# Kernel optimization log

Measured on AMD Instinct MI355X. Metric: run time of the kernel, lower is better.

The kernel has to match this reference:

```python
import jax, jax.numpy as jnp
import numpy as np

B, T, I, H, O = 64, 512, 256, 1024, 128

def setup_inputs() -> dict:
    key = jax.random.key(0)
    ks = jax.random.split(key, 7)
    s_ih = 1.0 / np.sqrt(H)
    return {
        "x":    jax.random.normal(ks[0], (B, T, I), dtype=jnp.float32),
        "W_ih": jax.random.uniform(ks[1], (H, I), minval=-s_ih, maxval=s_ih, dtype=jnp.float32),
        "W_hh": jax.random.uniform(ks[2], (H, H), minval=-s_ih, maxval=s_ih, dtype=jnp.float32),
        "b_ih": jax.random.uniform(ks[3], (H,), minval=-s_ih, maxval=s_ih, dtype=jnp.float32),
        "b_hh": jax.random.uniform(ks[4], (H,), minval=-s_ih, maxval=s_ih, dtype=jnp.float32),
        "W_lin": jax.random.uniform(ks[5], (O, H), minval=-s_ih, maxval=s_ih, dtype=jnp.float32),
        "b_lin": jax.random.uniform(ks[6], (O,), minval=-s_ih, maxval=s_ih, dtype=jnp.float32),
    }

def reference(x, W_ih, W_hh, b_ih, b_hh, W_lin, b_lin):
    # Precompute input projections for all timesteps: [T, B, H]
    xp = jnp.einsum('bti,hi->tbh', x, W_ih) + b_ih + b_hh
    h0 = jnp.zeros((x.shape[0], W_hh.shape[0]), dtype=x.dtype)

    def step(h, xp_t):
        h_new = jnp.tanh(xp_t + h @ W_hh.T)
        return h_new, None

    h_last, _ = jax.lax.scan(step, h0, xp)
    # Final linear on last hidden state: [B, O]
    return h_last @ W_lin.T + b_lin
```

## Files before the change

kernel.cpp:

```cpp
#include <hip/hip_runtime.h>
#include <cstdint>
#include <cstddef>

#define B_ 64
#define T_ 512
#define I_ 256
#define H_ 1024
#define O_ 128

#define NGRP  8
#define NSLC  8
#define GROWS 8
#define SCOLS 128

typedef __attribute__((ext_vector_type(8))) short short8;
typedef __attribute__((ext_vector_type(4))) float f32x4;

__device__ __forceinline__ unsigned short f2bf(float f) {
    union { float f; unsigned int u; } v; v.f = f;
    unsigned int r = v.u + 0x7fffu + ((v.u >> 16) & 1u);
    return (unsigned short)(r >> 16);
}
__device__ __forceinline__ float bf2f(unsigned short h) {
    union { float f; unsigned int u; } v; v.u = ((unsigned int)h) << 16;
    return v.f;
}
__device__ __forceinline__ short8 pack8(const float* p) {
    float4 a = *(const float4*)p;
    float4 b = *(const float4*)(p + 4);
    short8 r;
    r[0] = (short)f2bf(a.x); r[1] = (short)f2bf(a.y);
    r[2] = (short)f2bf(a.z); r[3] = (short)f2bf(a.w);
    r[4] = (short)f2bf(b.x); r[5] = (short)f2bf(b.y);
    r[6] = (short)f2bf(b.z); r[7] = (short)f2bf(b.w);
    return r;
}
__device__ __forceinline__ f32x4 zero4() {
    f32x4 v; v[0] = 0.f; v[1] = 0.f; v[2] = 0.f; v[3] = 0.f; return v;
}
__device__ __forceinline__ void vdrain() {
    asm volatile("s_waitcnt vmcnt(0)" ::: "memory");
}

#define XS 264

__global__ __launch_bounds__(256) void xproj_kernel(
        const float* __restrict__ x, const float* __restrict__ W_ih,
        const float* __restrict__ b_ih, const float* __restrict__ b_hh,
        unsigned short* __restrict__ xp) {
    const int ntile = blockIdx.x;
    const int tg    = blockIdx.y;
    const int tid   = threadIdx.x;
    const int wave  = tid >> 6, lane = tid & 63;
    const int m     = lane & 15, quad = lane >> 4;
    const int wrow  = (wave & 1) * 32;
    const int wcol  = (wave >> 1) * 32;

    __shared__ unsigned short lds_x[64 * XS];

    short8 bfr[2][8];
    float  bias[2];
    #pragma unroll
    for (int ct = 0; ct < 2; ++ct) {
        const int col = ntile * 64 + wcol + ct * 16 + m;
        bias[ct] = b_ih[col] + b_hh[col];
        #pragma unroll
        for (int ks = 0; ks < 8; ++ks)
            bfr[ct][ks] = pack8(W_ih + (size_t)col * I_ + ks * 32 + quad * 8);
    }

    for (int it = 0; it < 8; ++it) {
        const int t = tg * 8 + it;
        #pragma unroll
        for (int j = 0; j < 16; ++j) {
            const int row = j * 4 + wave;
            float4 v = *(const float4*)(x + ((size_t)row * T_ + t) * I_ + lane * 4);
            uint2 p;
            p.x = (unsigned)f2bf(v.x) | ((unsigned)f2bf(v.y) << 16);
            p.y = (unsigned)f2bf(v.z) | ((unsigned)f2bf(v.w) << 16);
            *(uint2*)(&lds_x[row * XS + lane * 4]) = p;
        }
        __syncthreads();

        f32x4 acc[2][2];
        #pragma unroll
        for (int i = 0; i < 2; ++i)
            #pragma unroll
            for (int j = 0; j < 2; ++j) acc[i][j] = zero4();

        #pragma unroll
        for (int ks = 0; ks < 8; ++ks) {
            const int kb = ks * 32 + quad * 8;
            short8 af[2];
            #pragma unroll
            for (int rt = 0; rt < 2; ++rt)
                af[rt] = *(const short8*)(&lds_x[(wrow + rt * 16 + m) * XS + kb]);
            #pragma unroll
            for (int rt = 0; rt < 2; ++rt)
                #pragma unroll
                for (int ct = 0; ct < 2; ++ct)
                    acc[rt][ct] = __builtin_amdgcn_mfma_f32_16x16x32_bf16(
                        af[rt], bfr[ct][ks], acc[rt][ct], 0, 0, 0);
        }

        #pragma unroll
        for (int ct = 0; ct < 2; ++ct) {
            const int col = ntile * 64 + wcol + ct * 16 + m;
            #pragma unroll
            for (int rt = 0; rt < 2; ++rt)
                #pragma unroll
                for (int r = 0; r < 4; ++r) {
                    const int bl = wrow + rt * 16 + quad * 4 + r;
                    xp[((size_t)t * B_ + bl) * H_ + col] =
                        f2bf(acc[rt][ct][r] + bias[ct]);
                }
        }
        __syncthreads();
    }
}

#define LDS_STRIDE 1032
#define PO_S 20
#define POLL_BOUND 4096

__global__ __launch_bounds__(512, 1) void rnn_kernel(
        const float* __restrict__ W_hh, const unsigned short* __restrict__ xp,
        unsigned short* __restrict__ hbuf, unsigned int* __restrict__ flags) {
    const int slice = blockIdx.x >> 3;
    const int group = blockIdx.x & 7;
    const int tid   = threadIdx.x;
    const int wave  = tid >> 6, lane = tid & 63;
    const int m     = lane & 15, quad = lane >> 4;
    const int col   = slice * SCOLS + wave * 16 + m;

    __shared__ unsigned short lds_h[GROWS * LDS_STRIDE];
    __shared__ unsigned short lds_po[8][GROWS * PO_S];

    short8 bfrag[32];
    #pragma unroll
    for (int ks = 0; ks < 32; ++ks)
        bfrag[ks] = pack8(W_hh + (size_t)col * H_ + ks * 32 + quad * 8);

    unsigned int* gflags = flags + group * 8;
    unsigned int* myflag = gflags + slice;
    const unsigned int* pollp = gflags + (lane & 7);
    unsigned short* lds_po_w = &lds_po[wave][0];

    const int srow = tid >> 6, useg = tid & 63;
    const int prow = lane >> 3, pseg = lane & 7;

    for (int t = 0; t < T_; ++t) {
        const unsigned short* hsrc = hbuf + (size_t)(t & 1) * (B_ * H_)
                                          + (size_t)group * GROWS * H_;
        unsigned short* hdst = hbuf + (size_t)((t + 1) & 1) * (B_ * H_);

        unsigned short xpv[4];
        {
            const unsigned short* xpp =
                xp + ((size_t)t * B_ + group * GROWS + (quad & 1) * 4) * H_ + col;
            #pragma unroll
            for (int r = 0; r < 4; ++r) xpv[r] = xpp[(size_t)r * H_];
        }

        if (t > 0) {
            if (wave == 0) {
                const unsigned target = (unsigned)t;
                int spins = 0;
                while (true) {
                    unsigned fv;
                    asm volatile(
                        "global_load_dword %0, %1, off sc0 sc1\n\t"
                        "s_waitcnt vmcnt(0)"
                        : "=v"(fv) : "v"(pollp) : "memory");
                    if (__ballot(fv >= target) == ~0ull) break;
                    if (++spins >= POLL_BOUND) break;
                }
            }
            __syncthreads();
        }

        {
            const unsigned short* rp = hsrc + (size_t)srow * H_;
            uint4 sv0, sv1;
            asm volatile("global_load_dwordx4 %0, %1, off sc0 sc1"
                         : "=v"(sv0) : "v"(rp + useg * 8) : "memory");
            asm volatile("global_load_dwordx4 %0, %1, off sc0 sc1"
                         : "=v"(sv1) : "v"(rp + (useg + 64) * 8) : "memory");
            vdrain();
            *(uint4*)(&lds_h[srow * LDS_STRIDE + useg * 8]) = sv0;
            *(uint4*)(&lds_h[srow * LDS_STRIDE + (useg + 64) * 8]) = sv1;
        }
        __syncthreads();

        f32x4 acc[4];
        #pragma unroll
        for (int j = 0; j < 4; ++j) acc[j] = zero4();
        #pragma unroll
        for (int ks = 0; ks < 32; ks += 4) {
            #pragma unroll
            for (int j = 0; j < 4; ++j) {
                short8 a = *(const short8*)(
                    &lds_h[(m & 7) * LDS_STRIDE + (ks + j) * 32 + quad * 8]);
                acc[j] = __builtin_amdgcn_mfma_f32_16x16x32_bf16(
                    a, bfrag[ks + j], acc[j], 0, 0, 0);
            }
        }

        if (quad < 2) {
            #pragma unroll
            for (int r = 0; r < 4; ++r) {
                float v = acc[0][r] + acc[1][r] + acc[2][r] + acc[3][r]
                        + bf2f(xpv[r]);
                v = tanhf(v);
                lds_po_w[(quad * 4 + r) * PO_S + m] = f2bf(v);
            }
        }
        {
            unsigned v = *(const unsigned*)(&lds_po_w[prow * PO_S + pseg * 2]);
            const void* p = hdst + (size_t)(group * GROWS + prow) * H_
                            + slice * SCOLS + wave * 16 + pseg * 2;
            asm volatile("global_store_dword %0, %1, off sc0 sc1"
                         :: "v"(p), "v"(v) : "memory");
            vdrain();
        }
        __syncthreads();
        if (tid == 0 && t < T_ - 1) {
            unsigned fv = (unsigned)(t + 1);
            asm volatile("global_store_dword %0, %1, off sc0 sc1"
                         :: "v"(myflag), "v"(fv) : "memory");
        }
    }
}

__global__ __launch_bounds__(256) void out_kernel(
        const unsigned short* __restrict__ hfinal, const float* __restrict__ W_lin,
        const float* __restrict__ b_lin, float* __restrict__ out) {
    const int gwave = (int)((blockIdx.x * 256 + threadIdx.x) >> 6);
    const int lane  = threadIdx.x & 63;
    const int b = gwave >> 7, o = gwave & 127;

    const unsigned short* hp = hfinal + (size_t)b * H_ + lane * 16;
    const float*          wp = W_lin  + (size_t)o * H_ + lane * 16;
    float s = 0.f;
    #pragma unroll
    for (int j = 0; j < 16; ++j) s += bf2f(hp[j]) * wp[j];
    #pragma unroll
    for (int d = 32; d > 0; d >>= 1) s += __shfl_down(s, d, 64);
    if (lane == 0) out[(size_t)b * O_ + o] = s + b_lin[o];
}

extern "C" void kernel_launch(void* const* d_in, const int* in_sizes, int n_in,
                              void* d_out, int out_size, void* d_ws, size_t ws_size,
                              hipStream_t stream) {
    const float* x     = (const float*)d_in[0];
    const float* W_ih  = (const float*)d_in[1];
    const float* W_hh  = (const float*)d_in[2];
    const float* b_ih  = (const float*)d_in[3];
    const float* b_hh  = (const float*)d_in[4];
    const float* W_lin = (const float*)d_in[5];
    const float* b_lin = (const float*)d_in[6];

    const size_t XP_ELEMS = (size_t)T_ * B_ * H_;
    unsigned short* xp    = (unsigned short*)d_ws;
    unsigned short* hbuf  = xp + XP_ELEMS;
    unsigned int*   flags = (unsigned int*)(hbuf + 2 * (size_t)B_ * H_);

    (void)hipMemsetAsync(hbuf, 0,
                         2 * (size_t)B_ * H_ * sizeof(unsigned short)
                         + NGRP * 64 * sizeof(unsigned int), stream);

    dim3 gA(H_ / 64, T_ / 8);
    xproj_kernel<<<gA, 256, 0, stream>>>(x, W_ih, b_ih, b_hh, xp);
    rnn_kernel<<<64, 512, 0, stream>>>(W_hh, xp, hbuf, flags);
    out_kernel<<<(B_ * O_) / 4, 256, 0, stream>>>(hbuf, W_lin, b_lin, (float*)d_out);
}
```

Before: 1.785 ms.

## Fuse input projection into persistent RNN kernel with double-buffered x staging

Removes the separate xproj kernel and its bf16 intermediate buffer (T*B*H). Each RNN block now computes its slice of x_t @ W_ih^T with MFMA every step, using W_ih fragments held in registers. It prefetches the next timestep's x rows into a double-buffered LDS tile alongside the h loads. This avoids writing and re-reading the intermediate and the extra launch, but adds per-step MFMA work and register pressure to the latency-bound recurrent loop.

```diff
diff --git a/kernel.cpp b/kernel.cpp
--- a/kernel.cpp
+++ b/kernel.cpp
@@ -42,89 +42,15 @@
     asm volatile("s_waitcnt vmcnt(0)" ::: "memory");
 }
 
-#define XS 264
-
-__global__ __launch_bounds__(256) void xproj_kernel(
-        const float* __restrict__ x, const float* __restrict__ W_ih,
-        const float* __restrict__ b_ih, const float* __restrict__ b_hh,
-        unsigned short* __restrict__ xp) {
-    const int ntile = blockIdx.x;
-    const int tg    = blockIdx.y;
-    const int tid   = threadIdx.x;
-    const int wave  = tid >> 6, lane = tid & 63;
-    const int m     = lane & 15, quad = lane >> 4;
-    const int wrow  = (wave & 1) * 32;
-    const int wcol  = (wave >> 1) * 32;
-
-    __shared__ unsigned short lds_x[64 * XS];
-
-    short8 bfr[2][8];
-    float  bias[2];
-    #pragma unroll
-    for (int ct = 0; ct < 2; ++ct) {
-        const int col = ntile * 64 + wcol + ct * 16 + m;
-        bias[ct] = b_ih[col] + b_hh[col];
-        #pragma unroll
-        for (int ks = 0; ks < 8; ++ks)
-            bfr[ct][ks] = pack8(W_ih + (size_t)col * I_ + ks * 32 + quad * 8);
-    }
-
-    for (int it = 0; it < 8; ++it) {
-        const int t = tg * 8 + it;
-        #pragma unroll
-        for (int j = 0; j < 16; ++j) {
-            const int row = j * 4 + wave;
-            float4 v = *(const float4*)(x + ((size_t)row * T_ + t) * I_ + lane * 4);
-            uint2 p;
-            p.x = (unsigned)f2bf(v.x) | ((unsigned)f2bf(v.y) << 16);
-            p.y = (unsigned)f2bf(v.z) | ((unsigned)f2bf(v.w) << 16);
-            *(uint2*)(&lds_x[row * XS + lane * 4]) = p;
-        }
-        __syncthreads();
-
-        f32x4 acc[2][2];
-        #pragma unroll
-        for (int i = 0; i < 2; ++i)
-            #pragma unroll
-            for (int j = 0; j < 2; ++j) acc[i][j] = zero4();
-
-        #pragma unroll
-        for (int ks = 0; ks < 8; ++ks) {
-            const int kb = ks * 32 + quad * 8;
-            short8 af[2];
-            #pragma unroll
-            for (int rt = 0; rt < 2; ++rt)
-                af[rt] = *(const short8*)(&lds_x[(wrow + rt * 16 + m) * XS + kb]);
-            #pragma unroll
-            for (int rt = 0; rt < 2; ++rt)
-                #pragma unroll
-                for (int ct = 0; ct < 2; ++ct)
-                    acc[rt][ct] = __builtin_amdgcn_mfma_f32_16x16x32_bf16(
-                        af[rt], bfr[ct][ks], acc[rt][ct], 0, 0, 0);
-        }
-
-        #pragma unroll
-        for (int ct = 0; ct < 2; ++ct) {
-            const int col = ntile * 64 + wcol + ct * 16 + m;
-            #pragma unroll
-            for (int rt = 0; rt < 2; ++rt)
-                #pragma unroll
-                for (int r = 0; r < 4; ++r) {
-                    const int bl = wrow + rt * 16 + quad * 4 + r;
-                    xp[((size_t)t * B_ + bl) * H_ + col] =
-                        f2bf(acc[rt][ct][r] + bias[ct]);
-                }
-        }
-        __syncthreads();
-    }
-}
-
 #define LDS_STRIDE 1032
+#define XSL 264
 #define PO_S 20
 #define POLL_BOUND 4096
 
 __global__ __launch_bounds__(512, 1) void rnn_kernel(
-        const float* __restrict__ W_hh, const unsigned short* __restrict__ xp,
+        const float* __restrict__ W_hh, const float* __restrict__ W_ih,
+        const float* __restrict__ b_ih, const float* __restrict__ b_hh,
+        const float* __restrict__ x,
         unsigned short* __restrict__ hbuf, unsigned int* __restrict__ flags) {
     const int slice = blockIdx.x >> 3;
     const int group = blockIdx.x & 7;
@@ -135,11 +61,17 @@
 
     __shared__ unsigned short lds_h[GROWS * LDS_STRIDE];
     __shared__ unsigned short lds_po[8][GROWS * PO_S];
+    __shared__ unsigned short lds_x2[2][GROWS * XSL];
 
     short8 bfrag[32];
     #pragma unroll
     for (int ks = 0; ks < 32; ++ks)
         bfrag[ks] = pack8(W_hh + (size_t)col * H_ + ks * 32 + quad * 8);
+    short8 bfragIH[8];
+    #pragma unroll
+    for (int ks = 0; ks < 8; ++ks)
+        bfragIH[ks] = pack8(W_ih + (size_t)col * I_ + ks * 32 + quad * 8);
+    const float biasc = b_ih[col] + b_hh[col];
 
     unsigned int* gflags = flags + group * 8;
     unsigned int* myflag = gflags + slice;
@@ -149,17 +81,28 @@
     const int srow = tid >> 6, useg = tid & 63;
     const int prow = lane >> 3, pseg = lane & 7;
 
+    {
+        float4 v = *(const float4*)(
+            x + ((size_t)(group * GROWS + srow) * T_ + 0) * I_ + useg * 4);
+        uint2 p;
+        p.x = (unsigned)f2bf(v.x) | ((unsigned)f2bf(v.y) << 16);
+        p.y = (unsigned)f2bf(v.z) | ((unsigned)f2bf(v.w) << 16);
+        *(uint2*)(&lds_x2[0][srow * XSL + useg * 4]) = p;
+    }
+    __syncthreads();
+
     for (int t = 0; t < T_; ++t) {
         const unsigned short* hsrc = hbuf + (size_t)(t & 1) * (B_ * H_)
                                           + (size_t)group * GROWS * H_;
         unsigned short* hdst = hbuf + (size_t)((t + 1) & 1) * (B_ * H_);
 
-        unsigned short xpv[4];
-        {
-            const unsigned short* xpp =
-                xp + ((size_t)t * B_ + group * GROWS + (quad & 1) * 4) * H_ + col;
-            #pragma unroll
-            for (int r = 0; r < 4; ++r) xpv[r] = xpp[(size_t)r * H_];
+        f32x4 axp = zero4();
+        #pragma unroll
+        for (int ks = 0; ks < 8; ++ks) {
+            short8 a = *(const short8*)(
+                &lds_x2[t & 1][(m & 7) * XSL + ks * 32 + quad * 8]);
+            axp = __builtin_amdgcn_mfma_f32_16x16x32_bf16(
+                a, bfragIH[ks], axp, 0, 0, 0);
         }
 
         if (t > 0) {
@@ -186,6 +129,15 @@
                          : "=v"(sv0) : "v"(rp + useg * 8) : "memory");
             asm volatile("global_load_dwordx4 %0, %1, off sc0 sc1"
                          : "=v"(sv1) : "v"(rp + (useg + 64) * 8) : "memory");
+            if (t + 1 < T_) {
+                float4 v = *(const float4*)(
+                    x + ((size_t)(group * GROWS + srow) * T_ + (t + 1)) * I_
+                      + useg * 4);
+                uint2 p;
+                p.x = (unsigned)f2bf(v.x) | ((unsigned)f2bf(v.y) << 16);
+                p.y = (unsigned)f2bf(v.z) | ((unsigned)f2bf(v.w) << 16);
+                *(uint2*)(&lds_x2[(t + 1) & 1][srow * XSL + useg * 4]) = p;
+            }
             vdrain();
             *(uint4*)(&lds_h[srow * LDS_STRIDE + useg * 8]) = sv0;
             *(uint4*)(&lds_h[srow * LDS_STRIDE + (useg + 64) * 8]) = sv1;
@@ -210,7 +162,7 @@
             #pragma unroll
             for (int r = 0; r < 4; ++r) {
                 float v = acc[0][r] + acc[1][r] + acc[2][r] + acc[3][r]
-                        + bf2f(xpv[r]);
+                        + axp[r] + biasc;
                 v = tanhf(v);
                 lds_po_w[(quad * 4 + r) * PO_S + m] = f2bf(v);
             }
@@ -260,17 +212,13 @@
     const float* W_lin = (const float*)d_in[5];
     const float* b_lin = (const float*)d_in[6];
 
-    const size_t XP_ELEMS = (size_t)T_ * B_ * H_;
-    unsigned short* xp    = (unsigned short*)d_ws;
-    unsigned short* hbuf  = xp + XP_ELEMS;
+    unsigned short* hbuf  = (unsigned short*)d_ws;
     unsigned int*   flags = (unsigned int*)(hbuf + 2 * (size_t)B_ * H_);
 
     (void)hipMemsetAsync(hbuf, 0,
                          2 * (size_t)B_ * H_ * sizeof(unsigned short)
                          + NGRP * 64 * sizeof(unsigned int), stream);
 
-    dim3 gA(H_ / 64, T_ / 8);
-    xproj_kernel<<<gA, 256, 0, stream>>>(x, W_ih, b_ih, b_hh, xp);
-    rnn_kernel<<<64, 512, 0, stream>>>(W_hh, xp, hbuf, flags);
+    rnn_kernel<<<64, 512, 0, stream>>>(W_hh, W_ih, b_ih, b_hh, x, hbuf, flags);
     out_kernel<<<(B_ * O_) / 4, 256, 0, stream>>>(hbuf, W_lin, b_lin, (float*)d_out);
 }
```

After: 1.731 ms. -3.0%, faster.
